# Optimization experiments

Measured on AMD Instinct MI355X. Metric: run time of the kernel, lower is better.

The kernel has to match this reference:

```python
import jax, jax.numpy as jnp
import numpy as np

DIM = 512
HEADS = 8
DIM_HEAD = 64
INNER = HEADS * DIM_HEAD
SCALE = DIM_HEAD ** -0.5


def setup_inputs() -> dict:
    key = jax.random.key(0)
    ks = jax.random.split(key, 6)
    x = jax.random.normal(ks[0], (8, 1024, DIM), dtype=jnp.float32)
    # nn.Linear(dim, inner, bias=False): y = x @ W.T ; store W as [out, in]
    wq = jax.random.normal(ks[1], (INNER, DIM), dtype=jnp.float32) * (DIM ** -0.5)
    wk = jax.random.normal(ks[2], (INNER, DIM), dtype=jnp.float32) * (DIM ** -0.5)
    wv = jax.random.normal(ks[3], (INNER, DIM), dtype=jnp.float32) * (DIM ** -0.5)
    wo = jax.random.normal(ks[4], (DIM, INNER), dtype=jnp.float32) * (INNER ** -0.5)
    bo = jax.random.normal(ks[5], (DIM,), dtype=jnp.float32) * 0.01
    return {"x": x, "wq": wq, "wk": wk, "wv": wv, "wo": wo, "bo": bo}


def reference(x, wq, wk, wv, wo, bo):
    b, n, _ = x.shape
    # QKV projections -> [b, h, n, d]
    def proj(w):
        return (x @ w.T).reshape(b, n, HEADS, DIM_HEAD).transpose(0, 2, 1, 3)
    q, k, v = proj(wq), proj(wk), proj(wv)
    dots = jnp.einsum('bhid,bhjd->bhij', q, k) * SCALE
    dots = jnp.clip(dots, 1e-6, 1.0)
    dots_exp = jnp.exp(dots)
    attn = dots_exp / jnp.sum(dots_exp, axis=-1, keepdims=True)
    out = jnp.einsum('bhij,bhjd->bhid', attn, v)  # [b,h,n,d]
    out = out.transpose(0, 2, 1, 3).reshape(b, n, INNER)
    return out @ wo.T + bo
```

## Files before the change

kernel.cpp:

```cpp
#include <hip/hip_runtime.h>
#include <hip/hip_fp16.h>

#define BATCH 8
#define SEQ   1024
#define DIM   512
#define HEADS 8
#define DHEAD 64
#define MTOT  (BATCH*SEQ)

typedef _Float16 f16x8 __attribute__((ext_vector_type(8)));
typedef _Float16 f16x4 __attribute__((ext_vector_type(4)));
typedef float    fx4   __attribute__((ext_vector_type(4)));

#define MFMA16 __builtin_amdgcn_mfma_f32_16x16x32_f16

__device__ __forceinline__ void gload16(const _Float16* g, _Float16* l) {
    __builtin_amdgcn_global_load_lds(
        (const __attribute__((address_space(1))) unsigned int*)g,
        (__attribute__((address_space(3))) unsigned int*)l, 16, 0, 0);
}

__global__ __launch_bounds__(256) void convert_k(
    const float* __restrict__ x,  const float* __restrict__ wq,
    const float* __restrict__ wk, const float* __restrict__ wv,
    const float* __restrict__ wo,
    _Float16* __restrict__ xb, _Float16* __restrict__ wqkvb,
    _Float16* __restrict__ wob)
{
    const int XU = (MTOT*DIM)/4;
    const int WU = (DIM*DIM)/4;
    int idx = blockIdx.x*256 + threadIdx.x;
    if (idx >= XU + 4*WU) return;
    const float* src; _Float16* dst;
    if (idx < XU) { src = x + idx*4; dst = xb + idx*4; }
    else {
        int t = idx - XU; int region = t >> 16; int off = (t & 65535)*4;
        if      (region == 0) { src = wq + off; dst = wqkvb + off; }
        else if (region == 1) { src = wk + off; dst = wqkvb + DIM*DIM + off; }
        else if (region == 2) { src = wv + off; dst = wqkvb + 2*DIM*DIM + off; }
        else                  { src = wo + off; dst = wob + off; }
    }
    float4 v = *(const float4*)src;
    f16x4 o = { (_Float16)v.x, (_Float16)v.y, (_Float16)v.z, (_Float16)v.w };
    *(f16x4*)dst = o;
}

__global__ __launch_bounds__(256,3) void qkv_proj(
    const _Float16* __restrict__ A, const _Float16* __restrict__ B,
    _Float16* __restrict__ Qb, _Float16* __restrict__ Kb,
    _Float16* __restrict__ VTb)
{
    __shared__ _Float16 lA[128*64];
    __shared__ _Float16 lB[128*64];
    const int tid = threadIdx.x;
    const int m0 = blockIdx.y*128, n0 = blockIdx.x*128;
    const int w = tid>>6, l = tid&63, lr = l&15, lq = l>>4;
    const int wr = w>>1, wc = w&1;
    const int srow = (l>>3);
    const int scol = ((l&7) ^ ((l>>3)&7))*8;
    const int sw = lr&7;
    fx4 acc[4][4] = {};

    for (int k0 = 0; k0 < DIM; k0 += 64) {
        __syncthreads();
#pragma unroll
        for (int t = 0; t < 4; t++) {
            int row = w*32 + t*8;
            gload16(&A[(size_t)(m0+row+srow)*DIM + k0 + scol], &lA[row*64]);
            gload16(&B[(size_t)(n0+row+srow)*DIM + k0 + scol], &lB[row*64]);
        }
        __syncthreads();
#pragma unroll
        for (int kb = 0; kb < 2; kb++) {
            f16x8 af[4], bf[4];
#pragma unroll
            for (int cb = 0; cb < 4; cb++)
                bf[cb] = *(const f16x8*)&lB[(wc*64+cb*16+lr)*64 + (((kb*4+lq)^sw))*8];
#pragma unroll
            for (int rb = 0; rb < 4; rb++)
                af[rb] = *(const f16x8*)&lA[(wr*64+rb*16+lr)*64 + (((kb*4+lq)^sw))*8];
#pragma unroll
            for (int rb = 0; rb < 4; rb++)
#pragma unroll
                for (int cb = 0; cb < 4; cb++)
                    acc[rb][cb] = MFMA16(af[rb], bf[cb], acc[rb][cb], 0,0,0);
        }
    }
    if (n0 >= 1024) {
#pragma unroll
        for (int rb = 0; rb < 4; rb++)
#pragma unroll
            for (int cb = 0; cb < 4; cb++) {
                int inner = (n0 - 1024) + wc*64 + cb*16 + lr;
                int h = inner >> 6, d = inner & 63;
                int m = m0 + wr*64 + rb*16 + lq*4;
                int b = m >> 10, n = m & 1023;
                f16x4 v4;
#pragma unroll
                for (int i = 0; i < 4; i++) v4[i] = (_Float16)acc[rb][cb][i];
                *(f16x4*)&VTb[((size_t)(b*HEADS+h)*DHEAD + d)*SEQ + n] = v4;
            }
    } else {
#pragma unroll
        for (int rb = 0; rb < 4; rb++)
#pragma unroll
            for (int cb = 0; cb < 4; cb++) {
                int nn = n0 + wc*64 + cb*16 + lr;
                int which = nn >> 9, inner = nn & 511, h = inner >> 6, d = inner & 63;
#pragma unroll
                for (int i = 0; i < 4; i++) {
                    int m = m0 + wr*64 + rb*16 + lq*4 + i;
                    int b = m >> 10, n = m & 1023;
                    float v = acc[rb][cb][i];
                    if (which == 0)
                        Qb[((b*HEADS+h)*SEQ + n)*DHEAD + d] = (_Float16)(v * 0.125f);
                    else
                        Kb[((b*HEADS+h)*SEQ + n)*DHEAD + d] = (_Float16)v;
                }
            }
    }
}

__global__ __launch_bounds__(256,3) void attn_k(
    const _Float16* __restrict__ Q, const _Float16* __restrict__ K,
    const _Float16* __restrict__ VT, _Float16* __restrict__ AO)
{
    __shared__ __align__(16) char smem[53248];
    _Float16* lK  = (_Float16*)smem;
    _Float16* lVT = (_Float16*)(smem + 16384);
    _Float16* lPT = (_Float16*)(smem + 32768);
    _Float16* oscr = (_Float16*)smem;
    float* lsumBuf = (float*)(smem + 32768);

    const int tid = threadIdx.x;
    const int w = tid>>6, l = tid&63, lr = l&15, lq = l>>4;
    const int sw = lr&7;
    const int bh = blockIdx.y, q0 = blockIdx.x*64;
    const int b = bh>>3, h = bh&7;
    const _Float16* Qp = Q  + (size_t)bh*SEQ*DHEAD;
    const _Float16* Kp = K  + (size_t)bh*SEQ*DHEAD;
    const _Float16* Vp = VT + (size_t)bh*DHEAD*SEQ;
    _Float16* lPw = lPT + w*2560;

    const int kst_r = (l>>3), kst_c = ((l&7) ^ ((l>>3)&7))*8;
    const int vst_r = (l>>4);

    f16x8 qf[4][2];
#pragma unroll
    for (int qg = 0; qg < 4; qg++)
#pragma unroll
        for (int kb = 0; kb < 2; kb++)
            qf[qg][kb] = *(const f16x8*)&Qp[(q0+qg*16+lr)*DHEAD + kb*32 + lq*8];

    fx4 O[4][4] = {};
    float lsum[4] = {};

    for (int kt = 0; kt < 8; kt++) {
        int k0 = kt*128;
        __syncthreads();
#pragma unroll
        for (int t = 0; t < 4; t++) {
            int rbase = w*32 + t*8;
            gload16(&Kp[(size_t)(k0+rbase+kst_r)*DHEAD + kst_c], &lK[rbase*64]);
        }
#pragma unroll
        for (int t = 0; t < 4; t++) {
            int rbase = w*16 + t*4;
            int r = rbase + vst_r;
            int g = (l&15) ^ (r&7);
            gload16(&Vp[(size_t)r*SEQ + k0 + g*8], &lVT[rbase*128]);
        }
        __syncthreads();

#pragma unroll
        for (int rb2 = 0; rb2 < 2; rb2++) {
            int jrow = w*32 + rb2*16 + lr;
            f16x8 kf0 = *(const f16x8*)&lK[jrow*64 + ((lq^sw))*8];
            f16x8 kf1 = *(const f16x8*)&lK[jrow*64 + (((4+lq)^sw))*8];
#pragma unroll
            for (int qg = 0; qg < 4; qg++) {
                fx4 s = {};
                s = MFMA16(kf0, qf[qg][0], s, 0,0,0);
                s = MFMA16(kf1, qf[qg][1], s, 0,0,0);
                f16x4 p4;
#pragma unroll
                for (int i = 0; i < 4; i++) {
                    float p = __expf(__builtin_amdgcn_fmed3f(s[i], 1e-6f, 1.0f));
                    lsum[qg] += p;
                    p4[i] = (_Float16)p;
                }
                *(f16x4*)&lPw[(qg*16+lr)*40 + rb2*16 + lq*4] = p4;
            }
        }
        f16x8 vf[4];
#pragma unroll
        for (int db = 0; db < 4; db++)
            vf[db] = *(const f16x8*)&lVT[(db*16+lr)*128 + (((w*4+lq)^sw))*8];
#pragma unroll
        for (int qg = 0; qg < 4; qg++) {
            f16x8 pf = *(const f16x8*)&lPw[(qg*16+lr)*40 + lq*8];
#pragma unroll
            for (int db = 0; db < 4; db++)
                O[db][qg] = MFMA16(vf[db], pf, O[db][qg], 0,0,0);
        }
    }

#pragma unroll
    for (int qg = 0; qg < 4; qg++) {
        lsum[qg] += __shfl_xor(lsum[qg], 16);
        lsum[qg] += __shfl_xor(lsum[qg], 32);
    }
    __syncthreads();
    if (lq == 0) {
#pragma unroll
        for (int qg = 0; qg < 4; qg++)
            lsumBuf[w*64 + qg*16 + lr] = lsum[qg];
    }
    if (w > 0) {
        _Float16* oo = oscr + (w-1)*4352;
#pragma unroll
        for (int db = 0; db < 4; db++)
#pragma unroll
            for (int qg = 0; qg < 4; qg++) {
                f16x4 t;
#pragma unroll
                for (int i = 0; i < 4; i++) t[i] = (_Float16)O[db][qg][i];
                *(f16x4*)&oo[(qg*16+lr)*68 + db*16 + lq*4] = t;
            }
    }
    __syncthreads();
    if (w == 0) {
#pragma unroll
        for (int qg = 0; qg < 4; qg++) {
            float tot = lsum[qg] + lsumBuf[64 + qg*16+lr]
                      + lsumBuf[128 + qg*16+lr] + lsumBuf[192 + qg*16+lr];
            float inv = 1.0f / tot;
            int q = q0 + qg*16 + lr;
            _Float16* aop = AO + ((size_t)(b*SEQ + q)*HEADS + h)*DHEAD;
#pragma unroll
            for (int db = 0; db < 4; db++) {
                fx4 o = O[db][qg];
#pragma unroll
                for (int ww = 1; ww < 4; ww++) {
                    f16x4 t = *(const f16x4*)
                        &oscr[(ww-1)*4352 + (qg*16+lr)*68 + db*16 + lq*4];
#pragma unroll
                    for (int i = 0; i < 4; i++) o[i] += (float)t[i];
                }
                f16x4 r;
#pragma unroll
                for (int i = 0; i < 4; i++) r[i] = (_Float16)(o[i] * inv);
                *(f16x4*)&aop[db*16 + lq*4] = r;
            }
        }
    }
}

__global__ __launch_bounds__(256,3) void out_proj(
    const _Float16* __restrict__ A, const _Float16* __restrict__ B,
    const float* __restrict__ bo, float* __restrict__ out)
{
    __shared__ _Float16 lA[128*64];
    __shared__ _Float16 lB[128*64];
    const int tid = threadIdx.x;
    const int m0 = blockIdx.y*128, n0 = blockIdx.x*128;
    const int w = tid>>6, l = tid&63, lr = l&15, lq = l>>4;
    const int wr = w>>1, wc = w&1;
    const int srow = (l>>3);
    const int scol = ((l&7) ^ ((l>>3)&7))*8;
    const int sw = lr&7;
    fx4 acc[4][4] = {};

    for (int k0 = 0; k0 < DIM; k0 += 64) {
        __syncthreads();
#pragma unroll
        for (int t = 0; t < 4; t++) {
            int row = w*32 + t*8;
            gload16(&A[(size_t)(m0+row+srow)*DIM + k0 + scol], &lA[row*64]);
            gload16(&B[(size_t)(n0+row+srow)*DIM + k0 + scol], &lB[row*64]);
        }
        __syncthreads();
#pragma unroll
        for (int kb = 0; kb < 2; kb++) {
            f16x8 af[4], bf[4];
#pragma unroll
            for (int cb = 0; cb < 4; cb++)
                bf[cb] = *(const f16x8*)&lB[(wc*64+cb*16+lr)*64 + (((kb*4+lq)^sw))*8];
#pragma unroll
            for (int rb = 0; rb < 4; rb++)
                af[rb] = *(const f16x8*)&lA[(wr*64+rb*16+lr)*64 + (((kb*4+lq)^sw))*8];
#pragma unroll
            for (int rb = 0; rb < 4; rb++)
#pragma unroll
                for (int cb = 0; cb < 4; cb++)
                    acc[rb][cb] = MFMA16(af[rb], bf[cb], acc[rb][cb], 0,0,0);
        }
    }
#pragma unroll
    for (int rb = 0; rb < 4; rb++)
#pragma unroll
        for (int cb = 0; cb < 4; cb++) {
            int nn = n0 + wc*64 + cb*16 + lr;
            float bias = bo[nn];
#pragma unroll
            for (int i = 0; i < 4; i++) {
                int m = m0 + wr*64 + rb*16 + lq*4 + i;
                out[(size_t)m*DIM + nn] = acc[rb][cb][i] + bias;
            }
        }
}

extern "C" void kernel_launch(void* const* d_in, const int* in_sizes, int n_in,
                              void* d_out, int out_size, void* d_ws, size_t ws_size,
                              hipStream_t stream)
{
    const float* x  = (const float*)d_in[0];
    const float* wq = (const float*)d_in[1];
    const float* wk = (const float*)d_in[2];
    const float* wv = (const float*)d_in[3];
    const float* wo = (const float*)d_in[4];
    const float* bo = (const float*)d_in[5];
    float* out = (float*)d_out;
    char* ws = (char*)d_ws;

    _Float16* xb    = (_Float16*)(ws);
    _Float16* wqkvb = (_Float16*)(ws + 8388608);
    _Float16* wob   = (_Float16*)(ws + 9961472);
    _Float16* Qb    = (_Float16*)(ws + 10485760);
    _Float16* Kb    = (_Float16*)(ws + 18874368);
    _Float16* VTb   = (_Float16*)(ws + 27262976);
    _Float16* attnb = (_Float16*)(ws);

    convert_k<<<5120, 256, 0, stream>>>(x, wq, wk, wv, wo, xb, wqkvb, wob);
    qkv_proj<<<dim3(12, 64), 256, 0, stream>>>(xb, wqkvb, Qb, Kb, VTb);
    attn_k<<<dim3(16, 64), 256, 0, stream>>>(Qb, Kb, VTb, attnb);
    out_proj<<<dim3(4, 64), 256, 0, stream>>>(attnb, wob, bo, out);
}
```

Before: 153.0 us.

## Transpose GEMM operands for vectorized epilogue stores and widen attention blocks to 512 threads

For the Q/K projection and the output projection, the weight and activation operands are swapped so each accumulator's four consecutive values run along the contiguous head-dim or output dimension. This allows packed f16x4 and float4 stores in place of scattered scalar stores. The attention kernel now uses 512 threads covering 128 queries per block. Two groups of four waves share each K/V tile in LDS, which halves per-block global loads and launches half as many blocks, at the cost of more LDS per block and possibly lower occupancy.

```diff
diff --git a/kernel.cpp b/kernel.cpp
--- a/kernel.cpp
+++ b/kernel.cpp
@@ -46,19 +46,25 @@
 }
 
 __global__ __launch_bounds__(256,3) void qkv_proj(
-    const _Float16* __restrict__ A, const _Float16* __restrict__ B,
+    const _Float16* __restrict__ X, const _Float16* __restrict__ W,
     _Float16* __restrict__ Qb, _Float16* __restrict__ Kb,
     _Float16* __restrict__ VTb)
 {
     __shared__ _Float16 lA[128*64];
     __shared__ _Float16 lB[128*64];
     const int tid = threadIdx.x;
-    const int m0 = blockIdx.y*128, n0 = blockIdx.x*128;
     const int w = tid>>6, l = tid&63, lr = l&15, lq = l>>4;
     const int wr = w>>1, wc = w&1;
     const int srow = (l>>3);
-    const int scol = ((l&7) ^ ((l>>3)&7))*8;
+    const int scol = ((l&7) ^ srow)*8;
     const int sw = lr&7;
+    const bool qk = blockIdx.x < 8;
+    const _Float16 *pA, *pB;
+    int m0, n0;
+    if (qk) { m0 = blockIdx.x*128; n0 = blockIdx.y*128;
+              pA = W + (size_t)m0*DIM; pB = X + (size_t)n0*DIM; }
+    else    { m0 = blockIdx.y*128; n0 = 1024 + (blockIdx.x-8)*128;
+              pA = X + (size_t)m0*DIM; pB = W + (size_t)n0*DIM; }
     fx4 acc[4][4] = {};
 
     for (int k0 = 0; k0 < DIM; k0 += 64) {
@@ -66,8 +72,8 @@
 #pragma unroll
         for (int t = 0; t < 4; t++) {
             int row = w*32 + t*8;
-            gload16(&A[(size_t)(m0+row+srow)*DIM + k0 + scol], &lA[row*64]);
-            gload16(&B[(size_t)(n0+row+srow)*DIM + k0 + scol], &lB[row*64]);
+            gload16(&pA[(size_t)(row+srow)*DIM + k0 + scol], &lA[row*64]);
+            gload16(&pB[(size_t)(row+srow)*DIM + k0 + scol], &lB[row*64]);
         }
         __syncthreads();
 #pragma unroll
@@ -86,7 +92,27 @@
                     acc[rb][cb] = MFMA16(af[rb], bf[cb], acc[rb][cb], 0,0,0);
         }
     }
-    if (n0 >= 1024) {
+    if (qk) {
+#pragma unroll
+        for (int rb = 0; rb < 4; rb++)
+#pragma unroll
+            for (int cb = 0; cb < 4; cb++) {
+                int od = m0 + wr*64 + rb*16 + lq*4;
+                int sq = n0 + wc*64 + cb*16 + lr;
+                int b = sq >> 10, n = sq & 1023;
+                int which = od >> 9, h = (od >> 6) & 7, d0 = od & 63;
+                f16x4 v4;
+                if (which == 0) {
+#pragma unroll
+                    for (int i = 0; i < 4; i++) v4[i] = (_Float16)(acc[rb][cb][i]*0.125f);
+                    *(f16x4*)&Qb[((size_t)(b*HEADS+h)*SEQ + n)*DHEAD + d0] = v4;
+                } else {
+#pragma unroll
+                    for (int i = 0; i < 4; i++) v4[i] = (_Float16)acc[rb][cb][i];
+                    *(f16x4*)&Kb[((size_t)(b*HEADS+h)*SEQ + n)*DHEAD + d0] = v4;
+                }
+            }
+    } else {
 #pragma unroll
         for (int rb = 0; rb < 4; rb++)
 #pragma unroll
@@ -100,49 +126,29 @@
                 for (int i = 0; i < 4; i++) v4[i] = (_Float16)acc[rb][cb][i];
                 *(f16x4*)&VTb[((size_t)(b*HEADS+h)*DHEAD + d)*SEQ + n] = v4;
             }
-    } else {
-#pragma unroll
-        for (int rb = 0; rb < 4; rb++)
-#pragma unroll
-            for (int cb = 0; cb < 4; cb++) {
-                int nn = n0 + wc*64 + cb*16 + lr;
-                int which = nn >> 9, inner = nn & 511, h = inner >> 6, d = inner & 63;
-#pragma unroll
-                for (int i = 0; i < 4; i++) {
-                    int m = m0 + wr*64 + rb*16 + lq*4 + i;
-                    int b = m >> 10, n = m & 1023;
-                    float v = acc[rb][cb][i];
-                    if (which == 0)
-                        Qb[((b*HEADS+h)*SEQ + n)*DHEAD + d] = (_Float16)(v * 0.125f);
-                    else
-                        Kb[((b*HEADS+h)*SEQ + n)*DHEAD + d] = (_Float16)v;
-                }
-            }
-    }
-}
-
-__global__ __launch_bounds__(256,3) void attn_k(
+    }
+}
+
+__global__ __launch_bounds__(512,4) void attn_k(
     const _Float16* __restrict__ Q, const _Float16* __restrict__ K,
     const _Float16* __restrict__ VT, _Float16* __restrict__ AO)
 {
-    __shared__ __align__(16) char smem[53248];
+    __shared__ __align__(16) char smem[81920];
     _Float16* lK  = (_Float16*)smem;
     _Float16* lVT = (_Float16*)(smem + 16384);
     _Float16* lPT = (_Float16*)(smem + 32768);
-    _Float16* oscr = (_Float16*)smem;
-    float* lsumBuf = (float*)(smem + 32768);
-
     const int tid = threadIdx.x;
     const int w = tid>>6, l = tid&63, lr = l&15, lq = l>>4;
+    const int qh = w>>2, jw = w&3;
     const int sw = lr&7;
-    const int bh = blockIdx.y, q0 = blockIdx.x*64;
+    const int bh = blockIdx.y, q0 = blockIdx.x*128;
     const int b = bh>>3, h = bh&7;
     const _Float16* Qp = Q  + (size_t)bh*SEQ*DHEAD;
     const _Float16* Kp = K  + (size_t)bh*SEQ*DHEAD;
     const _Float16* Vp = VT + (size_t)bh*DHEAD*SEQ;
-    _Float16* lPw = lPT + w*2560;
-
-    const int kst_r = (l>>3), kst_c = ((l&7) ^ ((l>>3)&7))*8;
+    _Float16* lPw = lPT + w*3072;
+
+    const int kst_r = (l>>3), kst_c = ((l&7) ^ (l>>3))*8;
     const int vst_r = (l>>4);
 
     f16x8 qf[4][2];
@@ -150,7 +156,7 @@
     for (int qg = 0; qg < 4; qg++)
 #pragma unroll
         for (int kb = 0; kb < 2; kb++)
-            qf[qg][kb] = *(const f16x8*)&Qp[(q0+qg*16+lr)*DHEAD + kb*32 + lq*8];
+            qf[qg][kb] = *(const f16x8*)&Qp[(q0+qh*64+qg*16+lr)*DHEAD + kb*32 + lq*8];
 
     fx4 O[4][4] = {};
     float lsum[4] = {};
@@ -159,13 +165,13 @@
         int k0 = kt*128;
         __syncthreads();
 #pragma unroll
-        for (int t = 0; t < 4; t++) {
-            int rbase = w*32 + t*8;
+        for (int t = 0; t < 2; t++) {
+            int rbase = w*16 + t*8;
             gload16(&Kp[(size_t)(k0+rbase+kst_r)*DHEAD + kst_c], &lK[rbase*64]);
         }
 #pragma unroll
-        for (int t = 0; t < 4; t++) {
-            int rbase = w*16 + t*4;
+        for (int t = 0; t < 2; t++) {
+            int rbase = w*8 + t*4;
             int r = rbase + vst_r;
             int g = (l&15) ^ (r&7);
             gload16(&Vp[(size_t)r*SEQ + k0 + g*8], &lVT[rbase*128]);
@@ -174,7 +180,7 @@
 
 #pragma unroll
         for (int rb2 = 0; rb2 < 2; rb2++) {
-            int jrow = w*32 + rb2*16 + lr;
+            int jrow = jw*32 + rb2*16 + lr;
             f16x8 kf0 = *(const f16x8*)&lK[jrow*64 + ((lq^sw))*8];
             f16x8 kf1 = *(const f16x8*)&lK[jrow*64 + (((4+lq)^sw))*8];
 #pragma unroll
@@ -189,16 +195,16 @@
                     lsum[qg] += p;
                     p4[i] = (_Float16)p;
                 }
-                *(f16x4*)&lPw[(qg*16+lr)*40 + rb2*16 + lq*4] = p4;
+                *(f16x4*)&lPw[(qg*16+lr)*48 + rb2*16 + lq*4] = p4;
             }
         }
         f16x8 vf[4];
 #pragma unroll
         for (int db = 0; db < 4; db++)
-            vf[db] = *(const f16x8*)&lVT[(db*16+lr)*128 + (((w*4+lq)^sw))*8];
+            vf[db] = *(const f16x8*)&lVT[(db*16+lr)*128 + (((jw*4+lq)^sw))*8];
 #pragma unroll
         for (int qg = 0; qg < 4; qg++) {
-            f16x8 pf = *(const f16x8*)&lPw[(qg*16+lr)*40 + lq*8];
+            f16x8 pf = *(const f16x8*)&lPw[(qg*16+lr)*48 + lq*8];
 #pragma unroll
             for (int db = 0; db < 4; db++)
                 O[db][qg] = MFMA16(vf[db], pf, O[db][qg], 0,0,0);
@@ -211,13 +217,15 @@
         lsum[qg] += __shfl_xor(lsum[qg], 32);
     }
     __syncthreads();
+    float* lsumBuf = (float*)(smem + 53248);
+    _Float16* oscr = (_Float16*)smem;
     if (lq == 0) {
 #pragma unroll
         for (int qg = 0; qg < 4; qg++)
             lsumBuf[w*64 + qg*16 + lr] = lsum[qg];
     }
-    if (w > 0) {
-        _Float16* oo = oscr + (w-1)*4352;
+    if (jw > 0) {
+        _Float16* oo = oscr + (size_t)(qh*3 + (jw-1))*4352;
 #pragma unroll
         for (int db = 0; db < 4; db++)
 #pragma unroll
@@ -229,13 +237,15 @@
             }
     }
     __syncthreads();
-    if (w == 0) {
+    if (jw == 0) {
 #pragma unroll
         for (int qg = 0; qg < 4; qg++) {
-            float tot = lsum[qg] + lsumBuf[64 + qg*16+lr]
-                      + lsumBuf[128 + qg*16+lr] + lsumBuf[192 + qg*16+lr];
+            float tot = lsum[qg]
+                      + lsumBuf[(qh*4+1)*64 + qg*16+lr]
+                      + lsumBuf[(qh*4+2)*64 + qg*16+lr]
+                      + lsumBuf[(qh*4+3)*64 + qg*16+lr];
             float inv = 1.0f / tot;
-            int q = q0 + qg*16 + lr;
+            int q = q0 + qh*64 + qg*16 + lr;
             _Float16* aop = AO + ((size_t)(b*SEQ + q)*HEADS + h)*DHEAD;
 #pragma unroll
             for (int db = 0; db < 4; db++) {
@@ -243,7 +253,7 @@
 #pragma unroll
                 for (int ww = 1; ww < 4; ww++) {
                     f16x4 t = *(const f16x4*)
-                        &oscr[(ww-1)*4352 + (qg*16+lr)*68 + db*16 + lq*4];
+                        &oscr[(size_t)(qh*3+ww-1)*4352 + (qg*16+lr)*68 + db*16 + lq*4];
 #pragma unroll
                     for (int i = 0; i < 4; i++) o[i] += (float)t[i];
                 }
@@ -257,18 +267,20 @@
 }
 
 __global__ __launch_bounds__(256,3) void out_proj(
-    const _Float16* __restrict__ A, const _Float16* __restrict__ B,
+    const _Float16* __restrict__ Wo, const _Float16* __restrict__ Ain,
     const float* __restrict__ bo, float* __restrict__ out)
 {
     __shared__ _Float16 lA[128*64];
     __shared__ _Float16 lB[128*64];
     const int tid = threadIdx.x;
-    const int m0 = blockIdx.y*128, n0 = blockIdx.x*128;
+    const int m0 = blockIdx.x*128, n0 = blockIdx.y*128;
     const int w = tid>>6, l = tid&63, lr = l&15, lq = l>>4;
     const int wr = w>>1, wc = w&1;
     const int srow = (l>>3);
-    const int scol = ((l&7) ^ ((l>>3)&7))*8;
+    const int scol = ((l&7) ^ srow)*8;
     const int sw = lr&7;
+    const _Float16* pA = Wo + (size_t)m0*DIM;
+    const _Float16* pB = Ain + (size_t)n0*DIM;
     fx4 acc[4][4] = {};
 
     for (int k0 = 0; k0 < DIM; k0 += 64) {
@@ -276,8 +288,8 @@
 #pragma unroll
         for (int t = 0; t < 4; t++) {
             int row = w*32 + t*8;
-            gload16(&A[(size_t)(m0+row+srow)*DIM + k0 + scol], &lA[row*64]);
-            gload16(&B[(size_t)(n0+row+srow)*DIM + k0 + scol], &lB[row*64]);
+            gload16(&pA[(size_t)(row+srow)*DIM + k0 + scol], &lA[row*64]);
+            gload16(&pB[(size_t)(row+srow)*DIM + k0 + scol], &lB[row*64]);
         }
         __syncthreads();
 #pragma unroll
@@ -300,13 +312,15 @@
     for (int rb = 0; rb < 4; rb++)
 #pragma unroll
         for (int cb = 0; cb < 4; cb++) {
-            int nn = n0 + wc*64 + cb*16 + lr;
-            float bias = bo[nn];
-#pragma unroll
-            for (int i = 0; i < 4; i++) {
-                int m = m0 + wr*64 + rb*16 + lq*4 + i;
-                out[(size_t)m*DIM + nn] = acc[rb][cb][i] + bias;
-            }
+            int od = m0 + wr*64 + rb*16 + lq*4;
+            int sq = n0 + wc*64 + cb*16 + lr;
+            float4 bias = *(const float4*)&bo[od];
+            float4 r;
+            r.x = acc[rb][cb][0] + bias.x;
+            r.y = acc[rb][cb][1] + bias.y;
+            r.z = acc[rb][cb][2] + bias.z;
+            r.w = acc[rb][cb][3] + bias.w;
+            *(float4*)&out[(size_t)sq*DIM + od] = r;
         }
 }
 
@@ -333,6 +347,6 @@
 
     convert_k<<<5120, 256, 0, stream>>>(x, wq, wk, wv, wo, xb, wqkvb, wob);
     qkv_proj<<<dim3(12, 64), 256, 0, stream>>>(xb, wqkvb, Qb, Kb, VTb);
-    attn_k<<<dim3(16, 64), 256, 0, stream>>>(Qb, Kb, VTb, attnb);
-    out_proj<<<dim3(4, 64), 256, 0, stream>>>(attnb, wob, bo, out);
-}
+    attn_k<<<dim3(8, 64), 512, 0, stream>>>(Qb, Kb, VTb, attnb);
+    out_proj<<<dim3(4, 64), 256, 0, stream>>>(wob, attnb, bo, out);
+}
```

After: 189.6 us. 1.24x slower.
